# Optimization experiments

Measured on AMD Instinct MI355X. Metric: run time of the kernel, lower is better.

The kernel has to match this reference:

```python
import jax, jax.numpy as jnp
import numpy as np

INPUT_DIM = 1024
HIDDEN_DIM = 64   # per-head dim
NUM_HEADS = 16
PROJ = HIDDEN_DIM * NUM_HEADS  # 1024


def setup_inputs() -> dict:
    key = jax.random.key(0)
    ks = jax.random.split(key, 9)
    s = 1.0 / np.sqrt(INPUT_DIM)
    x = jax.random.normal(ks[0], (4, 2048, INPUT_DIM), dtype=jnp.float32)
    # Linear weights stored [in, out] (math-equivalent to torch's W.T)
    Wq = jax.random.uniform(ks[1], (INPUT_DIM, PROJ), jnp.float32, -s, s)
    bq = jax.random.uniform(ks[2], (PROJ,), jnp.float32, -s, s)
    Wk = jax.random.uniform(ks[3], (INPUT_DIM, PROJ), jnp.float32, -s, s)
    bk = jax.random.uniform(ks[4], (PROJ,), jnp.float32, -s, s)
    Wv = jax.random.uniform(ks[5], (INPUT_DIM, PROJ), jnp.float32, -s, s)
    bv = jax.random.uniform(ks[6], (PROJ,), jnp.float32, -s, s)
    sf = 1.0 / np.sqrt(PROJ)
    Wf = jax.random.uniform(ks[7], (PROJ, HIDDEN_DIM), jnp.float32, -sf, sf)
    bf = jax.random.uniform(ks[8], (HIDDEN_DIM,), jnp.float32, -sf, sf)
    return {"x": x, "Wq": Wq, "bq": bq, "Wk": Wk, "bk": bk,
            "Wv": Wv, "bv": bv, "Wf": Wf, "bf": bf}


def reference(x, Wq, bq, Wk, bk, Wv, bv, Wf, bf):
    B, S, _ = x.shape
    def split_heads(t):  # [B,S,H*D] -> [B,H,S,D]
        return t.reshape(B, S, NUM_HEADS, HIDDEN_DIM).transpose(0, 2, 1, 3)
    q = split_heads(x @ Wq + bq)
    k = split_heads(x @ Wk + bk)
    v = split_heads(x @ Wv + bv)
    scale = 1.0 / jnp.sqrt(jnp.float32(HIDDEN_DIM))
    scores = jnp.einsum('bhqd,bhkd->bhqk', q, k) * scale  # [B,H,S,S]
    weights = jax.nn.softmax(scores, axis=-1)
    ctx = jnp.einsum('bhqk,bhkd->bhqd', weights, v)
    ctx = ctx.transpose(0, 2, 1, 3).reshape(B, S, PROJ)
    return ctx @ Wf + bf  # [B,S,HIDDEN_DIM]
```

## Files before the change

### kernel.cpp

```cpp
#include <hip/hip_runtime.h>
#include <math.h>

#define S_LEN 2048
#define NH 16
#define HD 64
#define DMODEL 1024
#define BATCH 4
#define M_TOT (BATCH * S_LEN)

typedef __attribute__((ext_vector_type(8))) short bf16x8;
typedef __attribute__((ext_vector_type(4))) float f32x4;

#define CK 0.18033688f

__device__ __forceinline__ unsigned short f2bf_rne(float f) {
    unsigned u = __float_as_uint(f);
    u += 0x7fffu + ((u >> 16) & 1u);
    return (unsigned short)(u >> 16);
}

__device__ __forceinline__ void gld16(unsigned short* lds, const unsigned short* g) {
    __builtin_amdgcn_global_load_lds(
        (const __attribute__((address_space(1))) void*)g,
        (__attribute__((address_space(3))) void*)lds, 16, 0, 0);
}

__global__ __launch_bounds__(256) void cvt_fused(
    const float* __restrict__ x,
    const float* __restrict__ Wq, const float* __restrict__ Wk,
    const float* __restrict__ Wv, const float* __restrict__ Wf,
    unsigned short* __restrict__ xb, unsigned short* __restrict__ WT)
{
    const int z = blockIdx.z;
    const int tid = threadIdx.x;

    if (z < 4) {
        if (z == 3 && blockIdx.x > 0) return;
        const float* W = (z == 0) ? Wq : (z == 1) ? Wk : (z == 2) ? Wv : Wf;
        const int ncol = (z == 3) ? 64 : DMODEL;
        unsigned short* out = WT + (size_t)z * DMODEL * DMODEL;

        __shared__ float Lt[64][65];
        const int r0 = blockIdx.y * 64;
        const int c0 = blockIdx.x * 64;

        #pragma unroll
        for (int p = 0; p < 4; p++) {
            int row = (tid >> 4) + p * 16;
            int c4 = (tid & 15) * 4;
            float4 v = *(const float4*)(W + (size_t)(r0 + row) * ncol + c0 + c4);
            Lt[row][c4 + 0] = v.x; Lt[row][c4 + 1] = v.y;
            Lt[row][c4 + 2] = v.z; Lt[row][c4 + 3] = v.w;
        }
        __syncthreads();
        #pragma unroll
        for (int p = 0; p < 4; p++) {
            int nr = (tid >> 4) + p * 16;
            int kc = (tid & 15) * 4;
            unsigned short t[4];
            #pragma unroll
            for (int j = 0; j < 4; j++) t[j] = f2bf_rne(Lt[kc + j][nr]);
            *(uint2*)(out + (size_t)(c0 + nr) * DMODEL + r0 + kc) = *(uint2*)t;
        }
    } else {
        const int gtid = (blockIdx.y * 16 + blockIdx.x) * 256 + tid;
        #pragma unroll
        for (int it = 0; it < 8; it++) {
            #pragma unroll
            for (int k = 0; k < 4; k++) {
                size_t i = ((size_t)((it * 4 + k) * 65536) + gtid) * 4;
                float4 v = *(const float4*)(x + i);
                unsigned short t[4];
                t[0] = f2bf_rne(v.x); t[1] = f2bf_rne(v.y);
                t[2] = f2bf_rne(v.z); t[3] = f2bf_rne(v.w);
                *(uint2*)(xb + i) = *(uint2*)t;
            }
        }
    }
}

__global__ __launch_bounds__(256) void qkv_gemm_mfma(
    const unsigned short* __restrict__ xb,
    const unsigned short* __restrict__ WT,
    const float* __restrict__ bq, const float* __restrict__ bk,
    const float* __restrict__ bv,
    unsigned short* __restrict__ Qb, unsigned short* __restrict__ Kb,
    unsigned short* __restrict__ Vtb)
{
    __shared__ __align__(16) unsigned short As[16 * 512];
    __shared__ __align__(16) unsigned short Bs[16 * 512];

    const int lin = blockIdx.x + 8 * (blockIdx.y + 64 * blockIdx.z);
    const int xcd = lin & 7;
    const int s   = lin >> 3;
    const int rb  = xcd * 8 + (s & 7);
    const int ocz = s >> 3;
    const int ocb = ocz & 7;
    const int z   = ocz >> 3;

    const unsigned short* Wz = WT + (size_t)z * DMODEL * DMODEL;
    const float* bias = (z == 0) ? bq : (z == 1) ? bk : bv;

    const int tid = threadIdx.x;
    const int lane = tid & 63, w = tid >> 6;
    const int quad = lane >> 4, l15 = lane & 15;
    const int wm = w & 1, wn = w >> 1;

    const int OC0 = ocb * 128;
    const int R0  = rb * 128;

    const unsigned short* gA0 = Wz + (size_t)(OC0 + w * 16 + l15) * DMODEL + quad * 8;
    const unsigned short* gA1 = gA0 + (size_t)64 * DMODEL;
    const unsigned short* gB0 = xb + (size_t)(R0 + w * 16 + l15) * DMODEL + quad * 8;
    const unsigned short* gB1 = gB0 + (size_t)64 * DMODEL;

    f32x4 acc[4][4];
    #pragma unroll
    for (int i = 0; i < 4; i++)
        #pragma unroll
        for (int j = 0; j < 4; j++)
            #pragma unroll
            for (int c = 0; c < 4; c++) acc[i][j][c] = 0.f;

    for (int k0 = 0; k0 < DMODEL; k0 += 64) {
        __syncthreads();
        gld16(As + ((w + 0) * 2 + 0) * 512, gA0 + k0);
        gld16(As + ((w + 0) * 2 + 1) * 512, gA0 + k0 + 32);
        gld16(As + ((w + 4) * 2 + 0) * 512, gA1 + k0);
        gld16(As + ((w + 4) * 2 + 1) * 512, gA1 + k0 + 32);
        gld16(Bs + ((w + 0) * 2 + 0) * 512, gB0 + k0);
        gld16(Bs + ((w + 0) * 2 + 1) * 512, gB0 + k0 + 32);
        gld16(Bs + ((w + 4) * 2 + 0) * 512, gB1 + k0);
        gld16(Bs + ((w + 4) * 2 + 1) * 512, gB1 + k0 + 32);
        __syncthreads();

        #pragma unroll
        for (int sl = 0; sl < 2; sl++) {
            bf16x8 af[4], bfr[4];
            #pragma unroll
            for (int t = 0; t < 4; t++) {
                af[t]  = *(const bf16x8*)&As[((wm * 4 + t) * 2 + sl) * 512 + lane * 8];
                bfr[t] = *(const bf16x8*)&Bs[((wn * 4 + t) * 2 + sl) * 512 + lane * 8];
            }
            if (z != 2) {
                #pragma unroll
                for (int mt = 0; mt < 4; mt++)
                    #pragma unroll
                    for (int nt = 0; nt < 4; nt++)
                        acc[mt][nt] = __builtin_amdgcn_mfma_f32_16x16x32_bf16(
                            af[mt], bfr[nt], acc[mt][nt], 0, 0, 0);
            } else {
                #pragma unroll
                for (int mt = 0; mt < 4; mt++)
                    #pragma unroll
                    for (int nt = 0; nt < 4; nt++)
                        acc[mt][nt] = __builtin_amdgcn_mfma_f32_16x16x32_bf16(
                            bfr[nt], af[mt], acc[mt][nt], 0, 0, 0);
            }
        }
    }

    if (z != 2) {
        unsigned short* out = (z == 0) ? Qb : Kb;
        const float qs = (z == 0) ? CK : 1.0f;
        #pragma unroll
        for (int mt = 0; mt < 4; mt++) {
            int oc = OC0 + wm * 64 + mt * 16 + quad * 4;
            float4 bv4 = *(const float4*)&bias[oc];
            #pragma unroll
            for (int nt = 0; nt < 4; nt++) {
                int row = R0 + wn * 64 + nt * 16 + l15;
                unsigned short t4[4];
                t4[0] = f2bf_rne((acc[mt][nt][0] + bv4.x) * qs);
                t4[1] = f2bf_rne((acc[mt][nt][1] + bv4.y) * qs);
                t4[2] = f2bf_rne((acc[mt][nt][2] + bv4.z) * qs);
                t4[3] = f2bf_rne((acc[mt][nt][3] + bv4.w) * qs);
                *(uint2*)(out + (size_t)row * DMODEL + oc) = *(uint2*)t4;
            }
        }
    } else {
        const int b = R0 >> 11;
        const int sbase = (R0 & 2047) + wn * 64;
        #pragma unroll
        for (int mt = 0; mt < 4; mt++) {
            int oc = OC0 + wm * 64 + mt * 16 + l15;
            float bvv = bias[oc];
            #pragma unroll
            for (int nt = 0; nt < 4; nt++) {
                int sq = sbase + nt * 16 + quad * 4;
                unsigned short t4[4];
                t4[0] = f2bf_rne(acc[mt][nt][0] + bvv);
                t4[1] = f2bf_rne(acc[mt][nt][1] + bvv);
                t4[2] = f2bf_rne(acc[mt][nt][2] + bvv);
                t4[3] = f2bf_rne(acc[mt][nt][3] + bvv);
                *(uint2*)(Vtb + (size_t)(b * DMODEL + oc) * S_LEN + sq) = *(uint2*)t4;
            }
        }
    }
}

__global__ __launch_bounds__(256, 4) void flash_attn_mfma(
    const unsigned short* __restrict__ Qg,
    const unsigned short* __restrict__ Kg,
    const unsigned short* __restrict__ Vtg,
    unsigned short* __restrict__ ctxb)
{
    __shared__ __align__(16) unsigned short Ks[16 * 512];
    __shared__ __align__(16) unsigned short Vs[16 * 512];
    __shared__ __align__(16) unsigned short Ps[8 * 512];

    const int tid  = threadIdx.x;
    const int lane = tid & 63, w = tid >> 6;
    const int quad = lane >> 4, l15 = lane & 15;

    const int lin = blockIdx.x + 16 * (blockIdx.y + 16 * blockIdx.z);
    const int xcd = lin & 7;
    const int s   = lin >> 3;
    const int bh  = xcd + 8 * (s >> 4);
    const int qblk = s & 15;
    const int b = bh >> 4, h = bh & 15;
    const int r0 = qblk * 128;

    bf16x8 qf[2][2];
    #pragma unroll
    for (int nt = 0; nt < 2; nt++)
        #pragma unroll
        for (int ds = 0; ds < 2; ds++)
            qf[nt][ds] = *(const bf16x8*)(Qg +
                (size_t)(b * S_LEN + r0 + w * 32 + nt * 16 + l15) * DMODEL +
                h * HD + ds * 32 + quad * 8);

    const unsigned short* gK = Kg + (size_t)(b * S_LEN + w * 16 + l15) * DMODEL + h * HD + quad * 8;
    const unsigned short* gV = Vtg + ((size_t)((b * NH + h) * HD + w * 16 + l15)) * S_LEN + quad * 8;

    f32x4 O[2][4], lsum[2];
    #pragma unroll
    for (int rt = 0; rt < 2; rt++) {
        #pragma unroll
        for (int c = 0; c < 4; c++) lsum[rt][c] = 0.f;
        #pragma unroll
        for (int dt = 0; dt < 4; dt++)
            #pragma unroll
            for (int c = 0; c < 4; c++) O[rt][dt][c] = 0.f;
    }

    f32x4 zero4;
    #pragma unroll
    for (int c = 0; c < 4; c++) zero4[c] = 0.f;
    bf16x8 ones;
    #pragma unroll
    for (int c = 0; c < 8; c++) ones[c] = (short)0x3F80;

    for (int st = 0; st < S_LEN / 128; st++) {
        __syncthreads();
        gld16(Ks + ((w + 0) * 2 + 0) * 512, gK);
        gld16(Ks + ((w + 0) * 2 + 1) * 512, gK + 32);
        gld16(Ks + ((w + 4) * 2 + 0) * 512, gK + (size_t)64 * DMODEL);
        gld16(Ks + ((w + 4) * 2 + 1) * 512, gK + (size_t)64 * DMODEL + 32);
        gld16(Vs + (w * 4 + 0) * 512, gV);
        gld16(Vs + (w * 4 + 1) * 512, gV + 32);
        gld16(Vs + (w * 4 + 2) * 512, gV + 64);
        gld16(Vs + (w * 4 + 3) * 512, gV + 96);
        gK += (size_t)128 * DMODEL;
        gV += 128;
        __syncthreads();

        #pragma unroll
        for (int r = 0; r < 4; r++) {
            f32x4 sc[2][2];
            {
                bf16x8 kf0 = *(const bf16x8*)&Ks[((r * 2 + 0) * 2 + 0) * 512 + lane * 8];
                bf16x8 kf1 = *(const bf16x8*)&Ks[((r * 2 + 1) * 2 + 0) * 512 + lane * 8];
                sc[0][0] = __builtin_amdgcn_mfma_f32_16x16x32_bf16(kf0, qf[0][0], zero4, 0, 0, 0);
                sc[0][1] = __builtin_amdgcn_mfma_f32_16x16x32_bf16(kf0, qf[1][0], zero4, 0, 0, 0);
                sc[1][0] = __builtin_amdgcn_mfma_f32_16x16x32_bf16(kf1, qf[0][0], zero4, 0, 0, 0);
                sc[1][1] = __builtin_amdgcn_mfma_f32_16x16x32_bf16(kf1, qf[1][0], zero4, 0, 0, 0);
                kf0 = *(const bf16x8*)&Ks[((r * 2 + 0) * 2 + 1) * 512 + lane * 8];
                kf1 = *(const bf16x8*)&Ks[((r * 2 + 1) * 2 + 1) * 512 + lane * 8];
                sc[0][0] = __builtin_amdgcn_mfma_f32_16x16x32_bf16(kf0, qf[0][1], sc[0][0], 0, 0, 0);
                sc[0][1] = __builtin_amdgcn_mfma_f32_16x16x32_bf16(kf0, qf[1][1], sc[0][1], 0, 0, 0);
                sc[1][0] = __builtin_amdgcn_mfma_f32_16x16x32_bf16(kf1, qf[0][1], sc[1][0], 0, 0, 0);
                sc[1][1] = __builtin_amdgcn_mfma_f32_16x16x32_bf16(kf1, qf[1][1], sc[1][1], 0, 0, 0);
            }

            #pragma unroll
            for (int nt = 0; nt < 2; nt++) {
                #pragma unroll
                for (int mt = 0; mt < 2; mt++) {
                    unsigned u[4];
                    #pragma unroll
                    for (int c = 0; c < 4; c++)
                        u[c] = __float_as_uint(__builtin_amdgcn_exp2f(sc[mt][nt][c]));
                    uint2 pk;
                    pk.x = __builtin_amdgcn_perm(u[1], u[0], 0x07060302u);
                    pk.y = __builtin_amdgcn_perm(u[3], u[2], 0x07060302u);
                    int off = (w * 2 + nt) * 512 + (mt * 2 + (quad >> 1)) * 128 +
                              l15 * 8 + (quad & 1) * 4;
                    *(uint2*)&Ps[off] = pk;
                }
            }

            bf16x8 pf0 = *(const bf16x8*)&Ps[(w * 2 + 0) * 512 + lane * 8];
            bf16x8 pf1 = *(const bf16x8*)&Ps[(w * 2 + 1) * 512 + lane * 8];
            lsum[0] = __builtin_amdgcn_mfma_f32_16x16x32_bf16(pf0, ones, lsum[0], 0, 0, 0);
            lsum[1] = __builtin_amdgcn_mfma_f32_16x16x32_bf16(pf1, ones, lsum[1], 0, 0, 0);
            #pragma unroll
            for (int dt = 0; dt < 4; dt++) {
                bf16x8 vf = *(const bf16x8*)&Vs[(dt * 4 + r) * 512 + lane * 8];
                O[0][dt] = __builtin_amdgcn_mfma_f32_16x16x32_bf16(pf0, vf, O[0][dt], 0, 0, 0);
                O[1][dt] = __builtin_amdgcn_mfma_f32_16x16x32_bf16(pf1, vf, O[1][dt], 0, 0, 0);
            }
        }
    }

    const size_t srow = (size_t)(b * S_LEN + r0 + w * 32);
    #pragma unroll
    for (int rt = 0; rt < 2; rt++) {
        #pragma unroll
        for (int reg = 0; reg < 4; reg++) {
            float li = 1.0f / lsum[rt][reg];
            size_t rowoff = (srow + rt * 16 + quad * 4 + reg) * DMODEL + h * HD + l15;
            #pragma unroll
            for (int dt = 0; dt < 4; dt++)
                ctxb[rowoff + dt * 16] = f2bf_rne(O[rt][dt][reg] * li);
        }
    }
}

__global__ __launch_bounds__(512) void out_proj_mfma(
    const unsigned short* __restrict__ ctxb,
    const unsigned short* __restrict__ WfT,
    const float* __restrict__ bfb,
    float* __restrict__ out)
{
    __shared__ float Red[8 * 1024];

    const int tid = threadIdx.x;
    const int lane = tid & 63, w = tid >> 6;
    const int quad = lane >> 4, l15 = lane & 15;
    const int m0 = blockIdx.x * 16;

    const unsigned short* pA = ctxb + (size_t)(m0 + l15) * DMODEL + w * 128 + quad * 8;
    const unsigned short* pB = WfT + (size_t)l15 * DMODEL + w * 128 + quad * 8;

    f32x4 acc[4];
    #pragma unroll
    for (int j = 0; j < 4; j++)
        #pragma unroll
        for (int c = 0; c < 4; c++) acc[j][c] = 0.f;

    #pragma unroll
    for (int k0 = 0; k0 < 128; k0 += 32) {
        bf16x8 af = *(const bf16x8*)(pA + k0);
        #pragma unroll
        for (int j = 0; j < 4; j++) {
            bf16x8 bfr = *(const bf16x8*)(pB + (size_t)j * 16 * DMODEL + k0);
            acc[j] = __builtin_amdgcn_mfma_f32_16x16x32_bf16(af, bfr, acc[j], 0, 0, 0);
        }
    }

    #pragma unroll
    for (int j = 0; j < 4; j++)
        #pragma unroll
        for (int reg = 0; reg < 4; reg++)
            Red[w * 1024 + lane * 16 + j * 4 + reg] = acc[j][reg];
    __syncthreads();

    const int row = tid >> 5;
    const int c0  = (tid & 31) * 2;
    float2 o;
    float* op = &o.x;
    #pragma unroll
    for (int cc = 0; cc < 2; cc++) {
        int col = c0 + cc;
        int idx = ((row >> 2) * 16 + (col & 15)) * 16 + (col >> 4) * 4 + (row & 3);
        float s = 0.f;
        #pragma unroll
        for (int wv = 0; wv < 8; wv++) s += Red[wv * 1024 + idx];
        op[cc] = s + bfb[col];
    }
    *(float2*)(out + (size_t)(m0 + row) * HD + c0) = o;
}

extern "C" void kernel_launch(void* const* d_in, const int* in_sizes, int n_in,
                              void* d_out, int out_size, void* d_ws, size_t ws_size,
                              hipStream_t stream)
{
    (void)in_sizes; (void)n_in; (void)out_size; (void)ws_size;
    const float* x  = (const float*)d_in[0];
    const float* Wq = (const float*)d_in[1];
    const float* bq = (const float*)d_in[2];
    const float* Wk = (const float*)d_in[3];
    const float* bk = (const float*)d_in[4];
    const float* Wv = (const float*)d_in[5];
    const float* bv = (const float*)d_in[6];
    const float* Wf = (const float*)d_in[7];
    const float* bf = (const float*)d_in[8];
    float* out = (float*)d_out;

    char* wsb = (char*)d_ws;
    unsigned short* xb   = (unsigned short*)wsb;
    unsigned short* ctxb = (unsigned short*)wsb;
    unsigned short* WT   = xb + (size_t)M_TOT * DMODEL;
    unsigned short* WfT  = WT + (size_t)3 * DMODEL * DMODEL;
    unsigned short* Qb   = (unsigned short*)(wsb + (size_t)32 * 1024 * 1024);
    unsigned short* Kb   = Qb + (size_t)M_TOT * DMODEL;
    unsigned short* Vtb  = Kb + (size_t)M_TOT * DMODEL;

    cvt_fused<<<dim3(16, 16, 5), 256, 0, stream>>>(x, Wq, Wk, Wv, Wf, xb, WT);
    qkv_gemm_mfma<<<dim3(8, 64, 3), 256, 0, stream>>>(xb, WT, bq, bk, bv, Qb, Kb, Vtb);
    flash_attn_mfma<<<dim3(S_LEN / 128, NH, BATCH), 256, 0, stream>>>(Qb, Kb, Vtb, ctxb);
    out_proj_mfma<<<dim3(M_TOT / 16), 512, 0, stream>>>(ctxb, WfT, bf, out);
}
```

Before: 286.3 us.

## Triple-buffer QKV GEMM loads and enlarge tile to 128x256 with 8 waves

Restructures the QKV projection GEMM to use 512-thread blocks covering 128 output columns by 256 rows, with a three-stage LDS ring of async global-to-LDS loads. Loads for tile t+2 are issued while tile t is computed, and explicit vmcnt waits plus raw s_barrier replace the double __syncthreads. MFMA sections run at raised wave priority. This aims to hide global memory latency and raise reuse of the weight tile. In exchange LDS use grows to about 144KB per block, which limits occupancy to one block per CU.

```diff
diff --git a/kernel.cpp b/kernel.cpp
--- a/kernel.cpp
+++ b/kernel.cpp
@@ -79,7 +79,7 @@
     }
 }
 
-__global__ __launch_bounds__(256) void qkv_gemm_mfma(
+__global__ __launch_bounds__(512) void qkv_gemm_mfma(
     const unsigned short* __restrict__ xb,
     const unsigned short* __restrict__ WT,
     const float* __restrict__ bq, const float* __restrict__ bk,
@@ -87,14 +87,14 @@
     unsigned short* __restrict__ Qb, unsigned short* __restrict__ Kb,
     unsigned short* __restrict__ Vtb)
 {
-    __shared__ __align__(16) unsigned short As[16 * 512];
-    __shared__ __align__(16) unsigned short Bs[16 * 512];
-
-    const int lin = blockIdx.x + 8 * (blockIdx.y + 64 * blockIdx.z);
+    __shared__ __align__(16) unsigned short As[3][16 * 512];
+    __shared__ __align__(16) unsigned short Bs[3][32 * 512];
+
+    const int lin = blockIdx.x;
     const int xcd = lin & 7;
     const int s   = lin >> 3;
-    const int rb  = xcd * 8 + (s & 7);
-    const int ocz = s >> 3;
+    const int rb  = xcd * 4 + (s & 3);
+    const int ocz = s >> 2;
     const int ocb = ocz & 7;
     const int z   = ocz >> 3;
 
@@ -104,15 +104,15 @@
     const int tid = threadIdx.x;
     const int lane = tid & 63, w = tid >> 6;
     const int quad = lane >> 4, l15 = lane & 15;
-    const int wm = w & 1, wn = w >> 1;
+    const int wq = w & 1;
+    const int wr = w >> 1;
 
     const int OC0 = ocb * 128;
-    const int R0  = rb * 128;
-
-    const unsigned short* gA0 = Wz + (size_t)(OC0 + w * 16 + l15) * DMODEL + quad * 8;
-    const unsigned short* gA1 = gA0 + (size_t)64 * DMODEL;
-    const unsigned short* gB0 = xb + (size_t)(R0 + w * 16 + l15) * DMODEL + quad * 8;
-    const unsigned short* gB1 = gB0 + (size_t)64 * DMODEL;
+    const int R0  = rb * 256;
+
+    const unsigned short* gA  = Wz + (size_t)(OC0 + w * 16 + l15) * DMODEL + quad * 8;
+    const unsigned short* gB0 = xb + (size_t)(R0  + w * 16 + l15) * DMODEL + quad * 8;
+    const unsigned short* gB1 = gB0 + (size_t)128 * DMODEL;
 
     f32x4 acc[4][4];
     #pragma unroll
@@ -122,77 +122,97 @@
             #pragma unroll
             for (int c = 0; c < 4; c++) acc[i][j][c] = 0.f;
 
-    for (int k0 = 0; k0 < DMODEL; k0 += 64) {
-        __syncthreads();
-        gld16(As + ((w + 0) * 2 + 0) * 512, gA0 + k0);
-        gld16(As + ((w + 0) * 2 + 1) * 512, gA0 + k0 + 32);
-        gld16(As + ((w + 4) * 2 + 0) * 512, gA1 + k0);
-        gld16(As + ((w + 4) * 2 + 1) * 512, gA1 + k0 + 32);
-        gld16(Bs + ((w + 0) * 2 + 0) * 512, gB0 + k0);
-        gld16(Bs + ((w + 0) * 2 + 1) * 512, gB0 + k0 + 32);
-        gld16(Bs + ((w + 4) * 2 + 0) * 512, gB1 + k0);
-        gld16(Bs + ((w + 4) * 2 + 1) * 512, gB1 + k0 + 32);
-        __syncthreads();
-
+#define QKV_STAGE(At, Bt, K)  do {                                 \
+        gld16((At) + (w * 2 + 0) * 512, gA  + (K));                \
+        gld16((At) + (w * 2 + 1) * 512, gA  + (K) + 32);           \
+        gld16((Bt) + (w * 2 + 0) * 512, gB0 + (K));                \
+        gld16((Bt) + (w * 2 + 1) * 512, gB0 + (K) + 32);           \
+        gld16((Bt) + ((w + 8) * 2 + 0) * 512, gB1 + (K));          \
+        gld16((Bt) + ((w + 8) * 2 + 1) * 512, gB1 + (K) + 32);     \
+    } while (0)
+
+    QKV_STAGE(As[0], Bs[0], 0);
+    QKV_STAGE(As[1], Bs[1], 64);
+
+    int cur = 0;
+    for (int t = 0; t < 16; ++t) {
+        if (t < 15) asm volatile("s_waitcnt vmcnt(6)" ::: "memory");
+        else        asm volatile("s_waitcnt vmcnt(0)" ::: "memory");
+        __builtin_amdgcn_s_barrier();
+
+        if (t <= 13) {
+            int nb = cur + 2; if (nb >= 3) nb -= 3;
+            QKV_STAGE(As[nb], Bs[nb], (t + 2) * 64);
+        }
+
+        const unsigned short* Ab = As[cur];
+        const unsigned short* Bb = Bs[cur];
+
+        __builtin_amdgcn_s_setprio(1);
         #pragma unroll
         for (int sl = 0; sl < 2; sl++) {
             bf16x8 af[4], bfr[4];
             #pragma unroll
-            for (int t = 0; t < 4; t++) {
-                af[t]  = *(const bf16x8*)&As[((wm * 4 + t) * 2 + sl) * 512 + lane * 8];
-                bfr[t] = *(const bf16x8*)&Bs[((wn * 4 + t) * 2 + sl) * 512 + lane * 8];
-            }
+            for (int i = 0; i < 4; i++)
+                af[i]  = *(const bf16x8*)&Ab[((wq * 4 + i) * 2 + sl) * 512 + lane * 8];
+            #pragma unroll
+            for (int j = 0; j < 4; j++)
+                bfr[j] = *(const bf16x8*)&Bb[((wr * 4 + j) * 2 + sl) * 512 + lane * 8];
             if (z != 2) {
                 #pragma unroll
-                for (int mt = 0; mt < 4; mt++)
+                for (int i = 0; i < 4; i++)
                     #pragma unroll
-                    for (int nt = 0; nt < 4; nt++)
-                        acc[mt][nt] = __builtin_amdgcn_mfma_f32_16x16x32_bf16(
-                            af[mt], bfr[nt], acc[mt][nt], 0, 0, 0);
+                    for (int j = 0; j < 4; j++)
+                        acc[i][j] = __builtin_amdgcn_mfma_f32_16x16x32_bf16(
+                            af[i], bfr[j], acc[i][j], 0, 0, 0);
             } else {
                 #pragma unroll
-                for (int mt = 0; mt < 4; mt++)
+                for (int i = 0; i < 4; i++)
                     #pragma unroll
-                    for (int nt = 0; nt < 4; nt++)
-                        acc[mt][nt] = __builtin_amdgcn_mfma_f32_16x16x32_bf16(
-                            bfr[nt], af[mt], acc[mt][nt], 0, 0, 0);
-            }
-        }
-    }
+                    for (int j = 0; j < 4; j++)
+                        acc[i][j] = __builtin_amdgcn_mfma_f32_16x16x32_bf16(
+                            bfr[j], af[i], acc[i][j], 0, 0, 0);
+            }
+        }
+        __builtin_amdgcn_s_setprio(0);
+
+        if (++cur == 3) cur = 0;
+    }
+#undef QKV_STAGE
 
     if (z != 2) {
         unsigned short* out = (z == 0) ? Qb : Kb;
         const float qs = (z == 0) ? CK : 1.0f;
         #pragma unroll
-        for (int mt = 0; mt < 4; mt++) {
-            int oc = OC0 + wm * 64 + mt * 16 + quad * 4;
+        for (int i = 0; i < 4; i++) {
+            int oc = OC0 + wq * 64 + i * 16 + quad * 4;
             float4 bv4 = *(const float4*)&bias[oc];
             #pragma unroll
-            for (int nt = 0; nt < 4; nt++) {
-                int row = R0 + wn * 64 + nt * 16 + l15;
+            for (int j = 0; j < 4; j++) {
+                int row = R0 + wr * 64 + j * 16 + l15;
                 unsigned short t4[4];
-                t4[0] = f2bf_rne((acc[mt][nt][0] + bv4.x) * qs);
-                t4[1] = f2bf_rne((acc[mt][nt][1] + bv4.y) * qs);
-                t4[2] = f2bf_rne((acc[mt][nt][2] + bv4.z) * qs);
-                t4[3] = f2bf_rne((acc[mt][nt][3] + bv4.w) * qs);
+                t4[0] = f2bf_rne((acc[i][j][0] + bv4.x) * qs);
+                t4[1] = f2bf_rne((acc[i][j][1] + bv4.y) * qs);
+                t4[2] = f2bf_rne((acc[i][j][2] + bv4.z) * qs);
+                t4[3] = f2bf_rne((acc[i][j][3] + bv4.w) * qs);
                 *(uint2*)(out + (size_t)row * DMODEL + oc) = *(uint2*)t4;
             }
         }
     } else {
         const int b = R0 >> 11;
-        const int sbase = (R0 & 2047) + wn * 64;
-        #pragma unroll
-        for (int mt = 0; mt < 4; mt++) {
-            int oc = OC0 + wm * 64 + mt * 16 + l15;
+        const int sbase = (R0 & 2047) + wr * 64;
+        #pragma unroll
+        for (int i = 0; i < 4; i++) {
+            int oc = OC0 + wq * 64 + i * 16 + l15;
             float bvv = bias[oc];
             #pragma unroll
-            for (int nt = 0; nt < 4; nt++) {
-                int sq = sbase + nt * 16 + quad * 4;
+            for (int j = 0; j < 4; j++) {
+                int sq = sbase + j * 16 + quad * 4;
                 unsigned short t4[4];
-                t4[0] = f2bf_rne(acc[mt][nt][0] + bvv);
-                t4[1] = f2bf_rne(acc[mt][nt][1] + bvv);
-                t4[2] = f2bf_rne(acc[mt][nt][2] + bvv);
-                t4[3] = f2bf_rne(acc[mt][nt][3] + bvv);
+                t4[0] = f2bf_rne(acc[i][j][0] + bvv);
+                t4[1] = f2bf_rne(acc[i][j][1] + bvv);
+                t4[2] = f2bf_rne(acc[i][j][2] + bvv);
+                t4[3] = f2bf_rne(acc[i][j][3] + bvv);
                 *(uint2*)(Vtb + (size_t)(b * DMODEL + oc) * S_LEN + sq) = *(uint2*)t4;
             }
         }
@@ -408,7 +428,7 @@
     unsigned short* Vtb  = Kb + (size_t)M_TOT * DMODEL;
 
     cvt_fused<<<dim3(16, 16, 5), 256, 0, stream>>>(x, Wq, Wk, Wv, Wf, xb, WT);
-    qkv_gemm_mfma<<<dim3(8, 64, 3), 256, 0, stream>>>(xb, WT, bq, bk, bv, Qb, Kb, Vtb);
+    qkv_gemm_mfma<<<dim3(768), 512, 0, stream>>>(xb, WT, bq, bk, bv, Qb, Kb, Vtb);
     flash_attn_mfma<<<dim3(S_LEN / 128, NH, BATCH), 256, 0, stream>>>(Qb, Kb, Vtb, ctxb);
     out_proj_mfma<<<dim3(M_TOT / 16), 512, 0, stream>>>(ctxb, WfT, bf, out);
 }
```

New measurement: 293.0 us. 1.02x slower.
